# Performance work log

Measured on AMD Instinct MI355X. Metric: run time of the kernel, lower is better.

## Reference

```python
import jax, jax.numpy as jnp
import numpy as np

B, T, D, H, HD = 2, 2048, 1024, 16, 64
EPS = 1.1920929e-07  # torch.finfo(float32).eps used by F.rms_norm default
VE_GATE_SCALE = 2.0
KEY_OFFSET = True


def rms_norm(x):
    return x * jax.lax.rsqrt(jnp.mean(x * x, axis=-1, keepdims=True) + EPS)


def apply_rotary(x, cos, sin):
    # x: [B,T,H,HD], cos/sin: [T, HD//2]
    c = cos[None, :, None, :]
    s = sin[None, :, None, :]
    x1, x2 = jnp.split(x, 2, axis=-1)
    return jnp.concatenate([x1 * c + x2 * s, -x1 * s + x2 * c], axis=-1)


def setup_inputs() -> dict:
    key = jax.random.key(0)
    ks = jax.random.split(key, 8)
    bound = (3.0 ** 0.5) * (D ** -0.5)
    x = jax.random.normal(ks[0], (B, T, D), dtype=jnp.float32)
    ve = jax.random.normal(ks[1], (B, T, H * HD), dtype=jnp.float32)
    sa_lambdas = jnp.ones((2,), dtype=jnp.float32)
    # realistic RoPE tables
    inv_freq = (10000.0 ** (-np.arange(HD // 2) / (HD // 2))).astype(np.float32)
    ang = np.arange(T, dtype=np.float32)[:, None] * inv_freq[None, :]
    cos = jnp.asarray(np.cos(ang))
    sin = jnp.asarray(np.sin(ang))
    # qkvo weight: uniform init everywhere (orig zeros o-proj; randomized for a non-trivial baseline)
    qkvo_w = jax.random.uniform(ks[2], (4 * D, D), dtype=jnp.float32, minval=-bound, maxval=bound)
    attn_gate_w = 0.02 * jax.random.normal(ks[3], (H, D), dtype=jnp.float32)
    ve_gate_w = 0.02 * jax.random.normal(ks[4], (H, D), dtype=jnp.float32)
    attn_scale = jnp.float32(0.12)
    docs = jnp.sort(jax.random.randint(ks[5], (T,), 0, 8).astype(jnp.int32))
    return {"x": x, "ve": ve, "sa_lambdas": sa_lambdas, "cos": cos, "sin": sin,
            "qkvo_w": qkvo_w, "attn_gate_w": attn_gate_w, "ve_gate_w": ve_gate_w,
            "attn_scale": attn_scale, "docs": docs}


def reference(x, ve, sa_lambdas, cos, sin, qkvo_w, attn_gate_w, ve_gate_w, attn_scale, docs):
    # QKV projection: rows [0:3D] of qkvo_w
    qkv = jnp.einsum('btd,ed->bte', x, sa_lambdas[0] * qkvo_w[:3 * D])
    qkv = qkv.reshape(B, T, 3 * H, HD)
    q, k, v = qkv[:, :, :H], qkv[:, :, H:2 * H], qkv[:, :, 2 * H:]
    q, k = rms_norm(q), rms_norm(k)
    q, k = apply_rotary(q, cos, sin), apply_rotary(k, cos, sin)
    if KEY_OFFSET:
        # shift two head-dim bands of k forward by one position
        k = k.at[:, 1:, :, HD // 4:HD // 2].set(k[:, :-1, :, HD // 4:HD // 2])
        k = k.at[:, 1:, :, 3 * HD // 4:].set(k[:, :-1, :, 3 * HD // 4:])
    # gated value embedding
    ve_gate = VE_GATE_SCALE * jax.nn.sigmoid(jnp.einsum('btd,hd->bth', x, ve_gate_w))
    v = v + ve_gate[..., None] * ve.reshape(B, T, H, HD)
    # causal + document masked attention (score_mod semantics)
    idx = jnp.arange(T)
    mask = (idx[:, None] >= idx[None, :]) & (docs[:, None] == docs[None, :])  # [T,T]
    scores = jnp.einsum('bqhd,bkhd->bhqk', q, k) * attn_scale
    scores = jnp.where(mask[None, None], scores, -jnp.inf)
    p = jax.nn.softmax(scores, axis=-1)
    y = jnp.einsum('bhqk,bkhd->bqhd', p, v)
    # attention output gate
    attn_gate = jax.nn.sigmoid(jnp.einsum('btd,hd->bth', x, attn_gate_w))
    y = y * attn_gate[..., None]
    # output projection: rows [3D:4D]
    y = y.reshape(B, T, H * HD)
    out = jnp.einsum('btd,ed->bte', y, sa_lambdas[1] * qkvo_w[3 * D:])
    return out
```

## Files before the change

### kernel.cpp

```cpp
#include <hip/hip_runtime.h>
#include <math.h>

#define B_ 2
#define T_ 2048
#define D_ 1024
#define H_ 16
#define HD_ 64
#define EPS_ 1.1920929e-07f
#define VE_SCALE_ 2.0f

#define NX4_ (B_ * T_ * D_ / 4)
#define NS4_ (3 * D_ * D_ / 4)
#define NQ4_ (4 * D_ * D_ / 4)
#define NG4_ (H_ * D_ / 4)

typedef __bf16 bf16_t;
typedef __bf16 bf16x4 __attribute__((ext_vector_type(4)));
typedef __bf16 bf16x8 __attribute__((ext_vector_type(8)));
typedef float f32x4 __attribute__((ext_vector_type(4)));

__device__ const f32x4 F4ZERO = {0.f, 0.f, 0.f, 0.f};

typedef __attribute__((address_space(1))) const void gvoid_t;
typedef __attribute__((address_space(3))) void lvoid_t;

__device__ __forceinline__ void gl_lds16(const bf16_t* g, bf16_t* l) {
  __builtin_amdgcn_global_load_lds((gvoid_t*)g, (lvoid_t*)l, 16, 0, 0);
}

__global__ __launch_bounds__(256) void cast_all(
    const float* __restrict__ x, const float* __restrict__ qkvo,
    const float* __restrict__ agw, const float* __restrict__ vgw,
    bf16_t* __restrict__ x_bf, bf16_t* __restrict__ wq,
    bf16_t* __restrict__ wo, bf16_t* __restrict__ wg)
{
  const int i = blockIdx.x * 256 + threadIdx.x;
  const float4* src;
  bf16x4* dst;
  if (i < NX4_) {
    src = (const float4*)x + i;
    dst = (bf16x4*)x_bf + i;
  } else if (i < NX4_ + NS4_) {
    const int j = i - NX4_;
    src = (const float4*)qkvo + j;
    dst = (bf16x4*)wq + j;
  } else if (i < NX4_ + NQ4_) {
    const int j = i - NX4_;
    src = (const float4*)qkvo + j;
    dst = (bf16x4*)wo + (j - NS4_);
  } else if (i < NX4_ + NQ4_ + NG4_) {
    const int j = i - NX4_ - NQ4_;
    src = (const float4*)agw + j;
    dst = (bf16x4*)wg + j;
  } else {
    const int j = i - NX4_ - NQ4_ - NG4_;
    src = (const float4*)vgw + j;
    dst = (bf16x4*)wg + NG4_ + j;
  }
  const float4 v = *src;
  bf16x4 o = {(bf16_t)v.x, (bf16_t)v.y, (bf16_t)v.z, (bf16_t)v.w};
  *dst = o;
}

__global__ __launch_bounds__(256) void gates_kernel(
    const bf16_t* __restrict__ x_bf, const bf16_t* __restrict__ wg,
    float* __restrict__ attn_gate, float* __restrict__ ve_gate2)
{
  const int bt = blockIdx.x;
  const int tid = threadIdx.x;
  __shared__ float xs[D_];
  {
    const bf16x4 xv = ((const bf16x4*)(x_bf + (size_t)bt * D_))[tid];
    xs[tid * 4 + 0] = (float)xv[0];
    xs[tid * 4 + 1] = (float)xv[1];
    xs[tid * 4 + 2] = (float)xv[2];
    xs[tid * 4 + 3] = (float)xv[3];
  }
  __syncthreads();
  const int g = tid >> 3, cg = tid & 7;
  const bf16x8* wrow = (const bf16x8*)(wg + (size_t)g * D_);
  float sum = 0.f;
#pragma unroll
  for (int j = 0; j < 16; ++j) {
    const bf16x8 w8 = wrow[cg + 8 * j];
    const float* xp = &xs[(cg + 8 * j) * 8];
#pragma unroll
    for (int e = 0; e < 8; ++e) sum = fmaf((float)w8[e], xp[e], sum);
  }
  sum += __shfl_xor(sum, 1);
  sum += __shfl_xor(sum, 2);
  sum += __shfl_xor(sum, 4);
  if (cg == 0) {
    const float sg = 1.f / (1.f + __expf(-sum));
    if (g < 16) attn_gate[bt * H_ + g] = sg;
    else        ve_gate2[bt * H_ + (g - 16)] = VE_SCALE_ * sg;
  }
}

__global__ __launch_bounds__(512) void gemm_qkv(
    const bf16_t* __restrict__ A, const bf16_t* __restrict__ W,
    const float* __restrict__ ve, const float* __restrict__ cosb,
    const float* __restrict__ sinb, const float* __restrict__ ve_gate2,
    bf16_t* __restrict__ q_bf, bf16_t* __restrict__ k_bf,
    bf16_t* __restrict__ v_bf, int K,
    const float* __restrict__ lam)
{
  const float scale = lam[0];
  __shared__ bf16_t As[2][128][32];
  __shared__ bf16_t Bs[2][128][32];
  const int tid = threadIdx.x;
  const int lane = tid & 63, w = tid >> 6;
  const int lr = lane & 15, lg = lane >> 4;
  const int wr = w >> 1, wc = w & 1;

  const int nwg = gridDim.x * gridDim.y;
  int bid = blockIdx.y * gridDim.x + blockIdx.x;
  bid = (bid & 7) * (nwg >> 3) + (bid >> 3);
  const int row0 = (bid / gridDim.x) * 128;
  const int col0 = (bid % gridDim.x) * 128;

  const int srow = w * 16 + (lane >> 2);
  const int scol = (lane & 3) * 8;
  const bf16_t* Ag = A + (size_t)(row0 + srow) * K + scol;
  const bf16_t* Wg = W + (size_t)(col0 + srow) * K + scol;

  f32x4 acc[2][4];
#pragma unroll
  for (int i = 0; i < 2; ++i)
#pragma unroll
    for (int j = 0; j < 4; ++j) acc[i][j] = F4ZERO;

#define STAGE_(bi, kk)                            \
  do {                                            \
    gl_lds16(Ag + (kk), &As[bi][w * 16][0]);      \
    gl_lds16(Wg + (kk), &Bs[bi][w * 16][0]);      \
  } while (0)

#define COMPUTE_(bi)                                                     \
  do {                                                                   \
    bf16x8 af[2], bfr[4];                                                \
    _Pragma("unroll")                                                    \
    for (int fm = 0; fm < 2; ++fm)                                       \
      af[fm] = *(const bf16x8*)&As[bi][wr * 32 + fm * 16 + lr][lg * 8];  \
    _Pragma("unroll")                                                    \
    for (int fn = 0; fn < 4; ++fn)                                       \
      bfr[fn] = *(const bf16x8*)&Bs[bi][wc * 64 + fn * 16 + lr][lg * 8]; \
    _Pragma("unroll")                                                    \
    for (int fm = 0; fm < 2; ++fm)                                       \
      _Pragma("unroll")                                                  \
      for (int fn = 0; fn < 4; ++fn)                                     \
        acc[fm][fn] = __builtin_amdgcn_mfma_f32_16x16x32_bf16(           \
            af[fm], bfr[fn], acc[fm][fn], 0, 0, 0);                      \
  } while (0)

  STAGE_(0, 0);
  __syncthreads();
  for (int k0 = 0; k0 + 64 <= K; k0 += 64) {
    STAGE_(1, k0 + 32);
    COMPUTE_(0);
    __syncthreads();
    if (k0 + 64 < K) STAGE_(0, k0 + 64);
    COMPUTE_(1);
    __syncthreads();
  }
#undef STAGE_
#undef COMPUTE_

  const int sec = col0 >> 10;
  const int h = ((col0 & 1023) >> 6) + wc;
#pragma unroll
  for (int fm = 0; fm < 2; ++fm) {
#pragma unroll
    for (int r = 0; r < 4; ++r) {
      const int row = row0 + wr * 32 + fm * 16 + lg * 4 + r;
      const int b = row >> 11, t = row & (T_ - 1);
      float v0 = acc[fm][0][r] * scale;
      float v1 = acc[fm][1][r] * scale;
      float v2 = acc[fm][2][r] * scale;
      float v3 = acc[fm][3][r] * scale;
      const size_t obase = ((size_t)(b * H_ + h) * T_ + t) * HD_;
      if (sec < 2) {
        float ssq = v0 * v0 + v1 * v1 + v2 * v2 + v3 * v3;
        ssq += __shfl_xor(ssq, 1);
        ssq += __shfl_xor(ssq, 2);
        ssq += __shfl_xor(ssq, 4);
        ssq += __shfl_xor(ssq, 8);
        const float rn = rsqrtf(ssq * (1.f / 64.f) + EPS_);
        v0 *= rn; v1 *= rn; v2 *= rn; v3 *= rn;
        const float c0 = cosb[t * 32 + lr], s0 = sinb[t * 32 + lr];
        const float c1 = cosb[t * 32 + 16 + lr], s1 = sinb[t * 32 + 16 + lr];
        const float o0 = fmaf(v0, c0, v2 * s0);
        const float o2 = fmaf(v2, c0, -v0 * s0);
        const float o1 = fmaf(v1, c1, v3 * s1);
        const float o3 = fmaf(v3, c1, -v1 * s1);
        bf16_t* dst = (sec == 0 ? q_bf : k_bf);
        dst[obase + 0 + lr]  = (bf16_t)o0;
        dst[obase + 16 + lr] = (bf16_t)o1;
        dst[obase + 32 + lr] = (bf16_t)o2;
        dst[obase + 48 + lr] = (bf16_t)o3;
      } else {
        const float g = ve_gate2[row * H_ + h];
        const float* vp = ve + (size_t)row * D_ + h * HD_;
        v0 = fmaf(g, vp[0 + lr], v0);
        v1 = fmaf(g, vp[16 + lr], v1);
        v2 = fmaf(g, vp[32 + lr], v2);
        v3 = fmaf(g, vp[48 + lr], v3);
        v_bf[obase + 0 + lr]  = (bf16_t)v0;
        v_bf[obase + 16 + lr] = (bf16_t)v1;
        v_bf[obase + 32 + lr] = (bf16_t)v2;
        v_bf[obase + 48 + lr] = (bf16_t)v3;
      }
    }
  }
}

__global__ __launch_bounds__(256) void gemm_bf16(
    const bf16_t* __restrict__ A, const bf16_t* __restrict__ W,
    float* __restrict__ Cout, int M, int N, int K,
    const float* __restrict__ lam, int li)
{
  const float scale = lam[li];
  __shared__ bf16_t As[2][64][32];
  __shared__ bf16_t Bs[2][128][32];
  const int tid = threadIdx.x;
  const int lane = tid & 63, w = tid >> 6;
  const int lr = lane & 15, lg = lane >> 4;
  const int wr = w >> 1, wc = w & 1;

  const int nwg = gridDim.x * gridDim.y;
  int bid = blockIdx.y * gridDim.x + blockIdx.x;
  bid = (bid & 7) * (nwg >> 3) + (bid >> 3);
  const int row0 = (bid / gridDim.x) * 64;
  const int col0 = (bid % gridDim.x) * 128;

  const int srow = lane >> 2;
  const int scol = (lane & 3) * 8;
  const bf16_t* Ag  = A + (size_t)(row0 + w * 16 + srow) * K + scol;
  const bf16_t* Wg0 = W + (size_t)(col0 + w * 16 + srow) * K + scol;
  const bf16_t* Wg1 = Wg0 + (size_t)64 * K;

  f32x4 acc[2][4];
#pragma unroll
  for (int i = 0; i < 2; ++i)
#pragma unroll
    for (int j = 0; j < 4; ++j) acc[i][j] = F4ZERO;

#define STAGE_(bi, kk)                                \
  do {                                                \
    gl_lds16(Ag + (kk), &As[bi][w * 16][0]);          \
    gl_lds16(Wg0 + (kk), &Bs[bi][w * 16][0]);         \
    gl_lds16(Wg1 + (kk), &Bs[bi][64 + w * 16][0]);    \
  } while (0)

#define COMPUTE_(bi)                                                     \
  do {                                                                   \
    bf16x8 af[2], bfr[4];                                                \
    _Pragma("unroll")                                                    \
    for (int fm = 0; fm < 2; ++fm)                                       \
      af[fm] = *(const bf16x8*)&As[bi][wr * 32 + fm * 16 + lr][lg * 8];  \
    _Pragma("unroll")                                                    \
    for (int fn = 0; fn < 4; ++fn)                                       \
      bfr[fn] = *(const bf16x8*)&Bs[bi][wc * 64 + fn * 16 + lr][lg * 8]; \
    _Pragma("unroll")                                                    \
    for (int fm = 0; fm < 2; ++fm)                                       \
      _Pragma("unroll")                                                  \
      for (int fn = 0; fn < 4; ++fn)                                     \
        acc[fm][fn] = __builtin_amdgcn_mfma_f32_16x16x32_bf16(           \
            af[fm], bfr[fn], acc[fm][fn], 0, 0, 0);                      \
  } while (0)

  STAGE_(0, 0);
  __syncthreads();
  for (int k0 = 0; k0 + 64 <= K; k0 += 64) {
    STAGE_(1, k0 + 32);
    COMPUTE_(0);
    __syncthreads();
    if (k0 + 64 < K) STAGE_(0, k0 + 64);
    COMPUTE_(1);
    __syncthreads();
  }
#undef STAGE_
#undef COMPUTE_

#pragma unroll
  for (int fm = 0; fm < 2; ++fm)
#pragma unroll
    for (int fn = 0; fn < 4; ++fn)
#pragma unroll
      for (int r = 0; r < 4; ++r) {
        const int row = row0 + wr * 32 + fm * 16 + lg * 4 + r;
        const int col = col0 + wc * 64 + fn * 16 + lr;
        Cout[(size_t)row * N + col] = acc[fm][fn][r] * scale;
      }
}

__global__ __launch_bounds__(256) void attn_mfma(
    const bf16_t* __restrict__ q_buf, const bf16_t* __restrict__ k_tmp,
    const bf16_t* __restrict__ v_buf, const float* __restrict__ attn_gate,
    const int* __restrict__ docs, const float* __restrict__ scale_ptr,
    bf16_t* __restrict__ y_buf)
{
  const int qt = blockIdx.x, bh = blockIdx.y;
  const int b = bh >> 4, h = bh & 15;
  const int tid = threadIdx.x;
  const int w = tid >> 6, lane = tid & 63;
  const int lr = lane & 15, lg = lane >> 4;
  const float scale = scale_ptr[0];
  __shared__ bf16_t Ks[64][72];
  __shared__ bf16_t Vt[64][72];
  __shared__ bf16_t Ps[64][72];
  __shared__ int dk[64];

  const int dlo = docs[qt * 64];
  const unsigned long long bal =
      __ballot((lane <= qt) && (docs[lane * 64 + 63] >= dlo));
  const int ktlo = __ffsll(bal) - 1;

  const bf16_t* qp = q_buf + ((size_t)bh * T_ + qt * 64 + w * 16 + lr) * HD_;
  const bf16x8 aq0 = *(const bf16x8*)(qp + lg * 8);
  const bf16x8 aq1 = *(const bf16x8*)(qp + 32 + lg * 8);
  int qpos_r[4], docq_r[4];
#pragma unroll
  for (int r = 0; r < 4; ++r) {
    qpos_r[r] = qt * 64 + w * 16 + lg * 4 + r;
    docq_r[r] = docs[qpos_r[r]];
  }
  f32x4 acc[4];
#pragma unroll
  for (int fn = 0; fn < 4; ++fn) acc[fn] = F4ZERO;
  float m[4] = {-1e30f, -1e30f, -1e30f, -1e30f};
  float l[4] = {0.f, 0.f, 0.f, 0.f};

#pragma unroll 1
  for (int kt = ktlo; kt <= qt; ++kt) {
    __syncthreads();
#pragma unroll
    for (int i = 0; i < 2; ++i) {
      const int idx = i * 256 + tid;
      const int krow = idx >> 3;
      const int c8 = (idx & 7) << 3;
      const int gk = kt * 64 + krow;
      const int gks = (((c8 & 16) != 0) && gk > 0) ? gk - 1 : gk;
      *(bf16x8*)&Ks[krow][c8] =
          *(const bf16x8*)(k_tmp + ((size_t)bh * T_ + gks) * HD_ + c8);
      const int kpos = idx & 63;
      const int d0 = (idx >> 6) << 3;
      const bf16x8 vv =
          *(const bf16x8*)(v_buf + ((size_t)bh * T_ + kt * 64 + kpos) * HD_ + d0);
#pragma unroll
      for (int j = 0; j < 8; ++j) Vt[d0 + j][kpos] = vv[j];
    }
    if (tid < 64) dk[tid] = docs[kt * 64 + tid];
    __syncthreads();

    f32x4 s[4];
#pragma unroll
    for (int fn = 0; fn < 4; ++fn) {
      const bf16x8 bk0 = *(const bf16x8*)&Ks[fn * 16 + lr][lg * 8];
      const bf16x8 bk1 = *(const bf16x8*)&Ks[fn * 16 + lr][32 + lg * 8];
      f32x4 z = F4ZERO;
      z = __builtin_amdgcn_mfma_f32_16x16x32_bf16(aq0, bk0, z, 0, 0, 0);
      s[fn] = __builtin_amdgcn_mfma_f32_16x16x32_bf16(aq1, bk1, z, 0, 0, 0);
    }
    const bool strict = (kt < qt);
#pragma unroll
    for (int fn = 0; fn < 4; ++fn) {
      const int kd = dk[fn * 16 + lr];
      const int kp = kt * 64 + fn * 16 + lr;
#pragma unroll
      for (int r = 0; r < 4; ++r) {
        const bool valid = (kd == docq_r[r]) && (strict || kp <= qpos_r[r]);
        s[fn][r] = valid ? s[fn][r] * scale : -3.0e38f;
      }
    }
#pragma unroll
    for (int r = 0; r < 4; ++r) {
      float cm = fmaxf(fmaxf(s[0][r], s[1][r]), fmaxf(s[2][r], s[3][r]));
      cm = fmaxf(cm, __shfl_xor(cm, 1));
      cm = fmaxf(cm, __shfl_xor(cm, 2));
      cm = fmaxf(cm, __shfl_xor(cm, 4));
      cm = fmaxf(cm, __shfl_xor(cm, 8));
      const float mn = fmaxf(m[r], cm);
      const float sc = __expf(m[r] - mn);
      m[r] = mn;
      const float p0 = __expf(s[0][r] - mn);
      const float p1 = __expf(s[1][r] - mn);
      const float p2 = __expf(s[2][r] - mn);
      const float p3 = __expf(s[3][r] - mn);
      float ps = (p0 + p1) + (p2 + p3);
      ps += __shfl_xor(ps, 1);
      ps += __shfl_xor(ps, 2);
      ps += __shfl_xor(ps, 4);
      ps += __shfl_xor(ps, 8);
      l[r] = l[r] * sc + ps;
      acc[0][r] *= sc; acc[1][r] *= sc; acc[2][r] *= sc; acc[3][r] *= sc;
      const int prow = w * 16 + lg * 4 + r;
      Ps[prow][0 + lr]  = (bf16_t)p0;
      Ps[prow][16 + lr] = (bf16_t)p1;
      Ps[prow][32 + lr] = (bf16_t)p2;
      Ps[prow][48 + lr] = (bf16_t)p3;
    }
    const bf16x8 ap0 = *(const bf16x8*)&Ps[w * 16 + lr][lg * 8];
    const bf16x8 ap1 = *(const bf16x8*)&Ps[w * 16 + lr][32 + lg * 8];
#pragma unroll
    for (int fn = 0; fn < 4; ++fn) {
      const bf16x8 bv0 = *(const bf16x8*)&Vt[fn * 16 + lr][lg * 8];
      const bf16x8 bv1 = *(const bf16x8*)&Vt[fn * 16 + lr][32 + lg * 8];
      acc[fn] = __builtin_amdgcn_mfma_f32_16x16x32_bf16(ap0, bv0, acc[fn], 0, 0, 0);
      acc[fn] = __builtin_amdgcn_mfma_f32_16x16x32_bf16(ap1, bv1, acc[fn], 0, 0, 0);
    }
  }
#pragma unroll
  for (int r = 0; r < 4; ++r) {
    const float inv = attn_gate[(size_t)(b * T_ + qpos_r[r]) * H_ + h] / l[r];
#pragma unroll
    for (int fn = 0; fn < 4; ++fn)
      y_buf[(size_t)(b * T_ + qpos_r[r]) * D_ + h * HD_ + fn * 16 + lr] =
          (bf16_t)(acc[fn][r] * inv);
  }
}

extern "C" void kernel_launch(void* const* d_in, const int* in_sizes, int n_in,
                              void* d_out, int out_size, void* d_ws, size_t ws_size,
                              hipStream_t stream) {
  const float* x    = (const float*)d_in[0];
  const float* ve   = (const float*)d_in[1];
  const float* lam  = (const float*)d_in[2];
  const float* cosb = (const float*)d_in[3];
  const float* sinb = (const float*)d_in[4];
  const float* qkvo = (const float*)d_in[5];
  const float* agw  = (const float*)d_in[6];
  const float* vgw  = (const float*)d_in[7];
  const float* ascl = (const float*)d_in[8];
  const int*   docs = (const int*)d_in[9];
  float* out = (float*)d_out;

  const size_t BT = (size_t)B_ * T_;
  float* cur = (float*)d_ws;
  bf16_t* x_bf = (bf16_t*)cur;        cur += BT * D_ / 2;
  bf16_t* wq_bf = (bf16_t*)cur;       cur += (size_t)3 * D_ * D_ / 2;
  bf16_t* wo_bf = (bf16_t*)cur;       cur += (size_t)D_ * D_ / 2;
  bf16_t* wg_bf = (bf16_t*)cur;       cur += (size_t)2 * H_ * D_ / 2;
  bf16_t* q_bf = (bf16_t*)cur;        cur += BT * D_ / 2;
  bf16_t* k_bf = (bf16_t*)cur;        cur += BT * D_ / 2;
  bf16_t* v_bf = (bf16_t*)cur;        cur += BT * D_ / 2;
  bf16_t* y_bf = (bf16_t*)cur;        cur += BT * D_ / 2;
  float* attn_gate = cur;             cur += BT * H_;
  float* ve_gate2 = cur;              cur += BT * H_;

  cast_all<<<(NX4_ + NQ4_ + 2 * NG4_) / 256, 256, 0, stream>>>(
      x, qkvo, agw, vgw, x_bf, wq_bf, wo_bf, wg_bf);

  gates_kernel<<<(int)BT, 256, 0, stream>>>(x_bf, wg_bf, attn_gate, ve_gate2);

  gemm_qkv<<<dim3(3 * D_ / 128, BT / 128), 512, 0, stream>>>(
      x_bf, wq_bf, ve, cosb, sinb, ve_gate2, q_bf, k_bf, v_bf, D_, lam);

  attn_mfma<<<dim3(T_ / 64, B_ * H_), 256, 0, stream>>>(
      q_bf, k_bf, v_bf, attn_gate, docs, ascl, y_bf);

  gemm_bf16<<<dim3(D_ / 128, BT / 64), 256, 0, stream>>>(
      y_bf, wo_bf, out, (int)BT, D_, D_, lam, 1);
}
```

Measured before the change: 114.5 us.

## Fuse cast and gate kernels; use eight waves in output projection GEMM

Merges the bf16 cast kernel and the gate-projection kernel into one launch, with extra blocks computing the sigmoid gates directly from fp32 x and fp32 gate weights. This removes a kernel launch and the separate casting of the gate weights. The output-projection GEMM moves from 4 to 8 waves per block, each wave owning a 32x32 sub-tile instead of 32x64. That raises parallelism inside the block, at the cost of fewer MFMAs per wave and more LDS fragment reads relative to compute. Gates now use fp32 x rather than bf16-rounded x, which slightly changes numerics.

```diff
diff --git a/kernel.cpp b/kernel.cpp
--- a/kernel.cpp
+++ b/kernel.cpp
@@ -12,7 +12,7 @@
 #define NX4_ (B_ * T_ * D_ / 4)
 #define NS4_ (3 * D_ * D_ / 4)
 #define NQ4_ (4 * D_ * D_ / 4)
-#define NG4_ (H_ * D_ / 4)
+#define CASTB_ ((NX4_ + NQ4_) / 256)
 
 typedef __bf16 bf16_t;
 typedef __bf16 bf16x4 __attribute__((ext_vector_type(4)));
@@ -28,64 +28,51 @@
   __builtin_amdgcn_global_load_lds((gvoid_t*)g, (lvoid_t*)l, 16, 0, 0);
 }
 
-__global__ __launch_bounds__(256) void cast_all(
+__global__ __launch_bounds__(256) void cast_gates(
     const float* __restrict__ x, const float* __restrict__ qkvo,
     const float* __restrict__ agw, const float* __restrict__ vgw,
     bf16_t* __restrict__ x_bf, bf16_t* __restrict__ wq,
-    bf16_t* __restrict__ wo, bf16_t* __restrict__ wg)
+    bf16_t* __restrict__ wo, float* __restrict__ attn_gate,
+    float* __restrict__ ve_gate2)
 {
-  const int i = blockIdx.x * 256 + threadIdx.x;
-  const float4* src;
-  bf16x4* dst;
-  if (i < NX4_) {
-    src = (const float4*)x + i;
-    dst = (bf16x4*)x_bf + i;
-  } else if (i < NX4_ + NS4_) {
-    const int j = i - NX4_;
-    src = (const float4*)qkvo + j;
-    dst = (bf16x4*)wq + j;
-  } else if (i < NX4_ + NQ4_) {
-    const int j = i - NX4_;
-    src = (const float4*)qkvo + j;
-    dst = (bf16x4*)wo + (j - NS4_);
-  } else if (i < NX4_ + NQ4_ + NG4_) {
-    const int j = i - NX4_ - NQ4_;
-    src = (const float4*)agw + j;
-    dst = (bf16x4*)wg + j;
-  } else {
-    const int j = i - NX4_ - NQ4_ - NG4_;
-    src = (const float4*)vgw + j;
-    dst = (bf16x4*)wg + NG4_ + j;
-  }
-  const float4 v = *src;
-  bf16x4 o = {(bf16_t)v.x, (bf16_t)v.y, (bf16_t)v.z, (bf16_t)v.w};
-  *dst = o;
-}
-
-__global__ __launch_bounds__(256) void gates_kernel(
-    const bf16_t* __restrict__ x_bf, const bf16_t* __restrict__ wg,
-    float* __restrict__ attn_gate, float* __restrict__ ve_gate2)
-{
-  const int bt = blockIdx.x;
+  __shared__ float xs[D_];
   const int tid = threadIdx.x;
-  __shared__ float xs[D_];
-  {
-    const bf16x4 xv = ((const bf16x4*)(x_bf + (size_t)bt * D_))[tid];
-    xs[tid * 4 + 0] = (float)xv[0];
-    xs[tid * 4 + 1] = (float)xv[1];
-    xs[tid * 4 + 2] = (float)xv[2];
-    xs[tid * 4 + 3] = (float)xv[3];
-  }
+  if (blockIdx.x < CASTB_) {
+    const int i = blockIdx.x * 256 + tid;
+    const float4* src;
+    bf16x4* dst;
+    if (i < NX4_) {
+      src = (const float4*)x + i;
+      dst = (bf16x4*)x_bf + i;
+    } else if (i < NX4_ + NS4_) {
+      const int j = i - NX4_;
+      src = (const float4*)qkvo + j;
+      dst = (bf16x4*)wq + j;
+    } else {
+      const int j = i - NX4_;
+      src = (const float4*)qkvo + j;
+      dst = (bf16x4*)wo + (j - NS4_);
+    }
+    const float4 v = *src;
+    bf16x4 o = {(bf16_t)v.x, (bf16_t)v.y, (bf16_t)v.z, (bf16_t)v.w};
+    *dst = o;
+    return;
+  }
+  const int bt = blockIdx.x - CASTB_;
+  *(float4*)&xs[tid * 4] = ((const float4*)(x + (size_t)bt * D_))[tid];
   __syncthreads();
   const int g = tid >> 3, cg = tid & 7;
-  const bf16x8* wrow = (const bf16x8*)(wg + (size_t)g * D_);
+  const float* wrow = (g < 16 ? agw + (size_t)g * D_
+                              : vgw + (size_t)(g - 16) * D_);
   float sum = 0.f;
 #pragma unroll
-  for (int j = 0; j < 16; ++j) {
-    const bf16x8 w8 = wrow[cg + 8 * j];
-    const float* xp = &xs[(cg + 8 * j) * 8];
-#pragma unroll
-    for (int e = 0; e < 8; ++e) sum = fmaf((float)w8[e], xp[e], sum);
+  for (int j = 0; j < 32; ++j) {
+    const float4 w4 = *(const float4*)(wrow + (cg + 8 * j) * 4);
+    const float* xp = &xs[(cg + 8 * j) * 4];
+    sum = fmaf(w4.x, xp[0], sum);
+    sum = fmaf(w4.y, xp[1], sum);
+    sum = fmaf(w4.z, xp[2], sum);
+    sum = fmaf(w4.w, xp[3], sum);
   }
   sum += __shfl_xor(sum, 1);
   sum += __shfl_xor(sum, 2);
@@ -214,7 +201,7 @@
   }
 }
 
-__global__ __launch_bounds__(256) void gemm_bf16(
+__global__ __launch_bounds__(512) void gemm_out(
     const bf16_t* __restrict__ A, const bf16_t* __restrict__ W,
     float* __restrict__ Cout, int M, int N, int K,
     const float* __restrict__ lam, int li)
@@ -225,7 +212,7 @@
   const int tid = threadIdx.x;
   const int lane = tid & 63, w = tid >> 6;
   const int lr = lane & 15, lg = lane >> 4;
-  const int wr = w >> 1, wc = w & 1;
+  const int wr = w >> 2, wc = w & 3;
 
   const int nwg = gridDim.x * gridDim.y;
   int bid = blockIdx.y * gridDim.x + blockIdx.x;
@@ -233,38 +220,37 @@
   const int row0 = (bid / gridDim.x) * 64;
   const int col0 = (bid % gridDim.x) * 128;
 
-  const int srow = lane >> 2;
+  const int srow = w * 16 + (lane >> 2);
+  const int srowA = (w & 3) * 16 + (lane >> 2);
   const int scol = (lane & 3) * 8;
-  const bf16_t* Ag  = A + (size_t)(row0 + w * 16 + srow) * K + scol;
-  const bf16_t* Wg0 = W + (size_t)(col0 + w * 16 + srow) * K + scol;
-  const bf16_t* Wg1 = Wg0 + (size_t)64 * K;
-
-  f32x4 acc[2][4];
+  const bf16_t* Ag = A + (size_t)(row0 + srowA) * K + scol;
+  const bf16_t* Wg = W + (size_t)(col0 + srow) * K + scol;
+
+  f32x4 acc[2][2];
 #pragma unroll
   for (int i = 0; i < 2; ++i)
 #pragma unroll
-    for (int j = 0; j < 4; ++j) acc[i][j] = F4ZERO;
-
-#define STAGE_(bi, kk)                                \
-  do {                                                \
-    gl_lds16(Ag + (kk), &As[bi][w * 16][0]);          \
-    gl_lds16(Wg0 + (kk), &Bs[bi][w * 16][0]);         \
-    gl_lds16(Wg1 + (kk), &Bs[bi][64 + w * 16][0]);    \
+    for (int j = 0; j < 2; ++j) acc[i][j] = F4ZERO;
+
+#define STAGE_(bi, kk)                                   \
+  do {                                                   \
+    gl_lds16(Wg + (kk), &Bs[bi][w * 16][0]);             \
+    if (w < 4) gl_lds16(Ag + (kk), &As[bi][(w & 3) * 16][0]); \
   } while (0)
 
 #define COMPUTE_(bi)                                                     \
   do {                                                                   \
-    bf16x8 af[2], bfr[4];                                                \
+    bf16x8 af[2], bfr[2];                                                \
     _Pragma("unroll")                                                    \
     for (int fm = 0; fm < 2; ++fm)                                       \
       af[fm] = *(const bf16x8*)&As[bi][wr * 32 + fm * 16 + lr][lg * 8];  \
     _Pragma("unroll")                                                    \
-    for (int fn = 0; fn < 4; ++fn)                                       \
-      bfr[fn] = *(const bf16x8*)&Bs[bi][wc * 64 + fn * 16 + lr][lg * 8]; \
+    for (int fn = 0; fn < 2; ++fn)                                       \
+      bfr[fn] = *(const bf16x8*)&Bs[bi][wc * 32 + fn * 16 + lr][lg * 8]; \
     _Pragma("unroll")                                                    \
     for (int fm = 0; fm < 2; ++fm)                                       \
       _Pragma("unroll")                                                  \
-      for (int fn = 0; fn < 4; ++fn)                                     \
+      for (int fn = 0; fn < 2; ++fn)                                     \
         acc[fm][fn] = __builtin_amdgcn_mfma_f32_16x16x32_bf16(           \
             af[fm], bfr[fn], acc[fm][fn], 0, 0, 0);                      \
   } while (0)
@@ -285,11 +271,11 @@
 #pragma unroll
   for (int fm = 0; fm < 2; ++fm)
 #pragma unroll
-    for (int fn = 0; fn < 4; ++fn)
+    for (int fn = 0; fn < 2; ++fn)
 #pragma unroll
       for (int r = 0; r < 4; ++r) {
         const int row = row0 + wr * 32 + fm * 16 + lg * 4 + r;
-        const int col = col0 + wc * 64 + fn * 16 + lr;
+        const int col = col0 + wc * 32 + fn * 16 + lr;
         Cout[(size_t)row * N + col] = acc[fm][fn][r] * scale;
       }
 }
@@ -440,7 +426,6 @@
   bf16_t* x_bf = (bf16_t*)cur;        cur += BT * D_ / 2;
   bf16_t* wq_bf = (bf16_t*)cur;       cur += (size_t)3 * D_ * D_ / 2;
   bf16_t* wo_bf = (bf16_t*)cur;       cur += (size_t)D_ * D_ / 2;
-  bf16_t* wg_bf = (bf16_t*)cur;       cur += (size_t)2 * H_ * D_ / 2;
   bf16_t* q_bf = (bf16_t*)cur;        cur += BT * D_ / 2;
   bf16_t* k_bf = (bf16_t*)cur;        cur += BT * D_ / 2;
   bf16_t* v_bf = (bf16_t*)cur;        cur += BT * D_ / 2;
@@ -448,10 +433,8 @@
   float* attn_gate = cur;             cur += BT * H_;
   float* ve_gate2 = cur;              cur += BT * H_;
 
-  cast_all<<<(NX4_ + NQ4_ + 2 * NG4_) / 256, 256, 0, stream>>>(
-      x, qkvo, agw, vgw, x_bf, wq_bf, wo_bf, wg_bf);
-
-  gates_kernel<<<(int)BT, 256, 0, stream>>>(x_bf, wg_bf, attn_gate, ve_gate2);
+  cast_gates<<<CASTB_ + (int)BT, 256, 0, stream>>>(
+      x, qkvo, agw, vgw, x_bf, wq_bf, wo_bf, attn_gate, ve_gate2);
 
   gemm_qkv<<<dim3(3 * D_ / 128, BT / 128), 512, 0, stream>>>(
       x_bf, wq_bf, ve, cosb, sinb, ve_gate2, q_bf, k_bf, v_bf, D_, lam);
@@ -459,6 +442,6 @@
   attn_mfma<<<dim3(T_ / 64, B_ * H_), 256, 0, stream>>>(
       q_bf, k_bf, v_bf, attn_gate, docs, ascl, y_bf);
 
-  gemm_bf16<<<dim3(D_ / 128, BT / 64), 256, 0, stream>>>(
+  gemm_out<<<dim3(D_ / 128, BT / 64), 512, 0, stream>>>(
       y_bf, wo_bf, out, (int)BT, D_, D_, lam, 1);
 }
```

New measurement: 119.6 us. +4.4%, slower.
